# Optimization experiments

Hardware: AMD Instinct MI355X
Metric: run time of the kernel (lower is better)

Reference implementation:

```python
import jax, jax.numpy as jnp
import numpy as np

B, C, NNEG, D = 4096, 5, 20, 128
NUM_EMB = 400000  # vocab * num_poly


def setup_inputs() -> dict:
    key = jax.random.key(0)
    k1, k2, k3, k4, k5 = jax.random.split(key, 5)
    iword = jax.random.randint(k1, (B,), 0, NUM_EMB, dtype=jnp.int64)
    owords = jax.random.randint(k2, (B, C), 0, NUM_EMB, dtype=jnp.int64)
    nwords = jax.random.randint(k3, (B, C * NNEG), 0, NUM_EMB, dtype=jnp.int64)
    emb1 = jax.random.normal(k4, (NUM_EMB, D), dtype=jnp.float32) * 0.1
    emb2 = jax.random.normal(k5, (NUM_EMB, D), dtype=jnp.float32) * 0.1
    return {"iword": iword, "owords": owords, "nwords": nwords,
            "emb1": emb1, "emb2": emb2}


def reference(iword, owords, nwords, emb1, emb2):
    v1 = emb1[iword]          # [B, D] center vectors
    v2 = emb2[owords]         # [B, C, D] context vectors
    vn = emb2[nwords]         # [B, C*NNEG, D] negative vectors
    # positive: mean over context of log sigmoid(v2 . v1)
    o_scores = jnp.einsum('bcd,bd->bc', v2, v1)
    oloss = jax.nn.log_sigmoid(o_scores).mean(axis=1)              # [B]
    # negatives: vectors are negated -> log sigmoid(-score), sum over negs, mean over context
    n_scores = jnp.einsum('bkd,bd->bk', vn, v1)                    # [B, C*NNEG]
    nloss = jax.nn.log_sigmoid(-n_scores).reshape(-1, C, NNEG).sum(axis=2).mean(axis=1)  # [B]
    return -(oloss + nloss).mean()
```

## Files before the change

### kernel.cpp

```cpp
#include <hip/hip_runtime.h>
#include <math.h>

#define B 4096
#define C 5
#define NNEG 20
#define D 128
#define NROWS (C + C * NNEG)
#define NSLOT 14

__device__ __forceinline__ float log_sigmoid(float x) {
    return fminf(x, 0.0f) - log1pf(__expf(-fabsf(x)));
}

__global__ __launch_bounds__(256) void sgns_partial(
    const int* __restrict__ iword,
    const int* __restrict__ owords,
    const int* __restrict__ nwords,
    const float* __restrict__ emb1,
    const float* __restrict__ emb2,
    float* __restrict__ partial)
{
    const int b    = blockIdx.x;
    const int tid  = threadIdx.x;
    const int lane = tid & 63;
    const int wave = tid >> 6;
    const int hw   = tid >> 5;
    const int l32  = tid & 31;

    const float4* v1p = (const float4*)(emb1 + (long)iword[b] * D);
    const float4 v1f = v1p[l32];

    int   rIdx[NSLOT];
    float sgn[NSLOT];
    bool  valid[NSLOT];
    #pragma unroll
    for (int s = 0; s < NSLOT; ++s) {
        const int r = s * 8 + hw;
        valid[s] = (r < NROWS);
        const int rr = valid[s] ? r : 0;
        const bool pos = (rr < C);
        sgn[s] = pos ? 1.0f : -1.0f;
        rIdx[s] = pos ? owords[b * C + rr]
                      : nwords[b * (C * NNEG) + (rr - C)];
    }

    float4 rw[NSLOT];
    #pragma unroll
    for (int s = 0; s < NSLOT; ++s) {
        rw[s] = ((const float4*)(emb2 + (long)rIdx[s] * D))[l32];
    }

    float acc = 0.0f;
    #pragma unroll
    for (int s = 0; s < NSLOT; ++s) {
        float t = v1f.x * rw[s].x + v1f.y * rw[s].y
                + v1f.z * rw[s].z + v1f.w * rw[s].w;
        t += __shfl_xor(t, 1, 64);
        t += __shfl_xor(t, 2, 64);
        t += __shfl_xor(t, 4, 64);
        t += __shfl_xor(t, 8, 64);
        t += __shfl_xor(t, 16, 64);
        const float v = log_sigmoid(sgn[s] * t);
        acc += valid[s] ? v : 0.0f;
    }

    acc += __shfl_xor(acc, 32, 64);

    __shared__ float wsum[4];
    if (lane == 0) wsum[wave] = acc;
    __syncthreads();
    if (tid == 0)
        partial[b] = wsum[0] + wsum[1] + wsum[2] + wsum[3];
}

__global__ __launch_bounds__(256) void sgns_reduce(
    const float* __restrict__ partial,
    float* __restrict__ out)
{
    const int tid = threadIdx.x;
    float acc = 0.0f;
    for (int i = tid; i < B; i += 256) acc += partial[i];

    #pragma unroll
    for (int off = 32; off > 0; off >>= 1)
        acc += __shfl_xor(acc, off, 64);

    __shared__ float ws[4];
    if ((tid & 63) == 0) ws[tid >> 6] = acc;
    __syncthreads();
    if (tid == 0) out[0] = -(ws[0] + ws[1] + ws[2] + ws[3]) / (float)(B * C);
}

extern "C" void kernel_launch(void* const* d_in, const int* in_sizes, int n_in,
                              void* d_out, int out_size, void* d_ws, size_t ws_size,
                              hipStream_t stream) {
    const int*   iword  = (const int*)d_in[0];
    const int*   owords = (const int*)d_in[1];
    const int*   nwords = (const int*)d_in[2];
    const float* emb1   = (const float*)d_in[3];
    const float* emb2   = (const float*)d_in[4];
    float* out     = (float*)d_out;
    float* partial = (float*)d_ws;

    sgns_partial<<<B, 256, 0, stream>>>(iword, owords, nwords, emb1, emb2, partial);
    sgns_reduce<<<1, 256, 0, stream>>>(partial, out);
}
```

Measured before the change: 361.2 us.

## Invert embedding gather into bucketed sequential stream over emb2 rows

Replaces the per-sample random gather of emb2 rows with a multi-kernel pipeline. First the center vectors are copied into a compact buffer. Then every (sample, row) lookup is scattered by atomics into per-row buckets of capacity 8, with an overflow list for rows that exceed it. Finally the whole emb2 table is streamed sequentially with one-row-ahead prefetch, and each row is dotted against the center vectors that requested it, with log-sigmoid and reductions done in separate kernels. This trades scattered HBM reads for a coalesced full-table scan, at the cost of atomics, extra launches and a score buffer. It falls back to the old gather when the workspace is too small.

```diff
diff --git a/kernel.cpp b/kernel.cpp
--- a/kernel.cpp
+++ b/kernel.cpp
@@ -6,64 +6,147 @@
 #define NNEG 20
 #define D 128
 #define NROWS (C + C * NNEG)
-#define NSLOT 14
+#define NEMB 400000
+#define CAP 8
+#define OVF_MAX 8192
+#define RPB 200
+#define SBLK (NEMB / RPB)
+#define NIT (RPB / 8)
+
+typedef unsigned int uint32;
+
+#define OFF_V1     ((size_t)0)
+#define OFF_SCORE  (OFF_V1 + (size_t)B * D * 4)
+#define OFF_PART   (OFF_SCORE + (size_t)B * NROWS * 4)
+#define OFF_CNT    (OFF_PART + (size_t)B * 4)
+#define OFF_OVFC   (OFF_CNT + (size_t)NEMB * 4)
+#define OFF_OVF    (OFF_OVFC + 64)
+#define OFF_BUCKET (OFF_OVF + (size_t)OVF_MAX * 8)
+#define WS_NEED    (OFF_BUCKET + (size_t)NEMB * CAP * 4)
 
 __device__ __forceinline__ float log_sigmoid(float x) {
     return fminf(x, 0.0f) - log1pf(__expf(-fabsf(x)));
 }
 
-__global__ __launch_bounds__(256) void sgns_partial(
-    const int* __restrict__ iword,
-    const int* __restrict__ owords,
-    const int* __restrict__ nwords,
-    const float* __restrict__ emb1,
-    const float* __restrict__ emb2,
-    float* __restrict__ partial)
-{
-    const int b    = blockIdx.x;
-    const int tid  = threadIdx.x;
-    const int lane = tid & 63;
-    const int wave = tid >> 6;
-    const int hw   = tid >> 5;
-    const int l32  = tid & 31;
-
-    const float4* v1p = (const float4*)(emb1 + (long)iword[b] * D);
-    const float4 v1f = v1p[l32];
-
-    int   rIdx[NSLOT];
-    float sgn[NSLOT];
-    bool  valid[NSLOT];
-    #pragma unroll
-    for (int s = 0; s < NSLOT; ++s) {
-        const int r = s * 8 + hw;
-        valid[s] = (r < NROWS);
-        const int rr = valid[s] ? r : 0;
-        const bool pos = (rr < C);
-        sgn[s] = pos ? 1.0f : -1.0f;
-        rIdx[s] = pos ? owords[b * C + rr]
-                      : nwords[b * (C * NNEG) + (rr - C)];
-    }
-
-    float4 rw[NSLOT];
-    #pragma unroll
-    for (int s = 0; s < NSLOT; ++s) {
-        rw[s] = ((const float4*)(emb2 + (long)rIdx[s] * D))[l32];
-    }
+__device__ __forceinline__ float dot_butterfly(float4 vf, float4 rv) {
+    float t = vf.x * rv.x + vf.y * rv.y + vf.z * rv.z + vf.w * rv.w;
+    t += __shfl_xor(t, 1, 64);
+    t += __shfl_xor(t, 2, 64);
+    t += __shfl_xor(t, 4, 64);
+    t += __shfl_xor(t, 8, 64);
+    t += __shfl_xor(t, 16, 64);
+    return t;
+}
+
+__global__ __launch_bounds__(256) void kA_init(const int* __restrict__ iword,
+                                               const float* __restrict__ emb1,
+                                               float* __restrict__ v1s,
+                                               uint32* __restrict__ cnt,
+                                               uint32* __restrict__ ovfc) {
+    const int g = blockIdx.x * 256 + threadIdx.x;
+    for (int i = g; i < NEMB; i += 512 * 256) cnt[i] = 0;
+    if (g == 0) *ovfc = 0;
+
+    const int hw = threadIdx.x >> 5, l32 = threadIdx.x & 31;
+    const int b = blockIdx.x * 8 + hw;
+    int ci = iword[b];
+    if ((unsigned)ci >= NEMB) ci = 0;
+    const float4 v = ((const float4*)(emb1 + (long)ci * D))[l32];
+    ((float4*)(v1s + (long)b * D))[l32] = v;
+}
+
+__global__ __launch_bounds__(128) void k2_scatter(const int* __restrict__ ow,
+                                                  const int* __restrict__ nw,
+                                                  uint32* __restrict__ cnt,
+                                                  uint32* __restrict__ bucket,
+                                                  uint32* __restrict__ ovfc,
+                                                  uint32* __restrict__ ovf) {
+    const int b = blockIdx.x;
+    const int r = threadIdx.x;
+    if (r >= NROWS) return;
+    int row = (r < C) ? ow[b * C + r] : nw[b * (C * NNEG) + (r - C)];
+    if ((unsigned)row >= NEMB) row = 0;
+    const uint32 pair = ((uint32)b << 7) | (uint32)r;
+    const uint32 c = atomicAdd(&cnt[row], 1u);
+    if (c < CAP) {
+        bucket[(long)row * CAP + c] = pair;
+    } else {
+        const uint32 o = atomicAdd(ovfc, 1u);
+        if (o < OVF_MAX) { ovf[2 * o] = (uint32)row; ovf[2 * o + 1] = pair; }
+    }
+}
+
+__global__ __launch_bounds__(256) void k3_stream(const float* __restrict__ emb2,
+                                                 const float* __restrict__ v1s,
+                                                 const uint32* __restrict__ cnt,
+                                                 const uint32* __restrict__ bucket,
+                                                 const uint32* __restrict__ ovfc,
+                                                 const uint32* __restrict__ ovf,
+                                                 float* __restrict__ score) {
+    const int tid = threadIdx.x;
+    const int hw = tid >> 5, l32 = tid & 31;
+    const int rbase = blockIdx.x * RPB;
+
+    int    row_c = rbase + hw;
+    float4 rv_c  = ((const float4*)(emb2 + (long)row_c * D))[l32];
+    uint32 n_c   = cnt[row_c];
+    uint32 bw_c  = bucket[(long)row_c * CAP + (l32 & 7)];
+
+    #pragma unroll 1
+    for (int i = 0; i < NIT; ++i) {
+        const int row_n = (i + 1 < NIT) ? (row_c + 8) : row_c;
+        const float4 rv_n = ((const float4*)(emb2 + (long)row_n * D))[l32];
+        const uint32 n_n  = cnt[row_n];
+        const uint32 bw_n = bucket[(long)row_n * CAP + (l32 & 7)];
+
+        if (n_c) {
+            uint32 n = n_c > CAP ? CAP : n_c;
+            for (uint32 k = 0; k < n; ++k) {
+                const uint32 pair = __shfl(bw_c, (int)k, 32);
+                const int bb = (int)(pair >> 7);
+                const int rr = (int)(pair & 127);
+                const float4 vf = ((const float4*)(v1s + (long)bb * D))[l32];
+                const float t = dot_butterfly(vf, rv_c);
+                if (l32 == 0 && bb < B && rr < NROWS) score[bb * NROWS + rr] = t;
+            }
+        }
+        row_c = row_n; rv_c = rv_n; n_c = n_n; bw_c = bw_n;
+    }
+
+    if (blockIdx.x == 0) {
+        uint32 m = *ovfc;
+        if (m > OVF_MAX) m = OVF_MAX;
+        for (uint32 e = hw; e < m; e += 8) {
+            uint32 row = ovf[2 * e];
+            const uint32 pair = ovf[2 * e + 1];
+            if (row >= NEMB) continue;
+            const int bb = (int)(pair >> 7);
+            const int rr = (int)(pair & 127);
+            const float4 rv = ((const float4*)(emb2 + (long)row * D))[l32];
+            const float4 vf = ((const float4*)(v1s + (long)bb * D))[l32];
+            const float t = dot_butterfly(vf, rv);
+            if (l32 == 0 && bb < B && rr < NROWS) score[bb * NROWS + rr] = t;
+        }
+    }
+}
+
+__global__ __launch_bounds__(256) void k5_finish(const float* __restrict__ score,
+                                                 float* __restrict__ partial) {
+    const int b = blockIdx.x;
+    const int tid = threadIdx.x;
+    const int lane = tid & 63, wave = tid >> 6, hw = tid >> 5;
 
     float acc = 0.0f;
     #pragma unroll
-    for (int s = 0; s < NSLOT; ++s) {
-        float t = v1f.x * rw[s].x + v1f.y * rw[s].y
-                + v1f.z * rw[s].z + v1f.w * rw[s].w;
-        t += __shfl_xor(t, 1, 64);
-        t += __shfl_xor(t, 2, 64);
-        t += __shfl_xor(t, 4, 64);
-        t += __shfl_xor(t, 8, 64);
-        t += __shfl_xor(t, 16, 64);
-        const float v = log_sigmoid(sgn[s] * t);
-        acc += valid[s] ? v : 0.0f;
-    }
-
+    for (int s = 0; s < 14; ++s) {
+        const int r = s * 8 + hw;
+        const bool valid = (r < NROWS);
+        const int rr = valid ? r : 0;
+        const float sgn = (rr < C) ? 1.0f : -1.0f;
+        const float t = score[b * NROWS + rr];
+        const float v = log_sigmoid(sgn * t);
+        acc += valid ? v : 0.0f;
+    }
     acc += __shfl_xor(acc, 32, 64);
 
     __shared__ float wsum[4];
@@ -73,22 +156,46 @@
         partial[b] = wsum[0] + wsum[1] + wsum[2] + wsum[3];
 }
 
-__global__ __launch_bounds__(256) void sgns_reduce(
-    const float* __restrict__ partial,
-    float* __restrict__ out)
-{
+__global__ __launch_bounds__(256) void sgns_reduce(const float* __restrict__ partial,
+                                                   float* __restrict__ out) {
     const int tid = threadIdx.x;
     float acc = 0.0f;
     for (int i = tid; i < B; i += 256) acc += partial[i];
-
     #pragma unroll
     for (int off = 32; off > 0; off >>= 1)
         acc += __shfl_xor(acc, off, 64);
-
     __shared__ float ws[4];
     if ((tid & 63) == 0) ws[tid >> 6] = acc;
     __syncthreads();
     if (tid == 0) out[0] = -(ws[0] + ws[1] + ws[2] + ws[3]) / (float)(B * C);
+}
+
+__global__ __launch_bounds__(256) void sgns_partial_gather(
+    const int* __restrict__ iword, const int* __restrict__ owords,
+    const int* __restrict__ nwords, const float* __restrict__ emb1,
+    const float* __restrict__ emb2, float* __restrict__ partial)
+{
+    const int b = blockIdx.x, tid = threadIdx.x;
+    const int lane = tid & 63, wave = tid >> 6, hw = tid >> 5, l32 = tid & 31;
+    const float4 v1f = ((const float4*)(emb1 + (long)iword[b] * D))[l32];
+    float acc = 0.0f;
+    #pragma unroll
+    for (int s = 0; s < 14; ++s) {
+        const int r = s * 8 + hw;
+        const bool valid = (r < NROWS);
+        const int rr = valid ? r : 0;
+        const bool pos = (rr < C);
+        const int idx = pos ? owords[b * C + rr] : nwords[b * (C * NNEG) + (rr - C)];
+        const float4 rv = ((const float4*)(emb2 + (long)idx * D))[l32];
+        const float t = dot_butterfly(v1f, rv);
+        const float v = log_sigmoid((pos ? 1.0f : -1.0f) * t);
+        acc += valid ? v : 0.0f;
+    }
+    acc += __shfl_xor(acc, 32, 64);
+    __shared__ float wsum[4];
+    if (lane == 0) wsum[wave] = acc;
+    __syncthreads();
+    if (tid == 0) partial[b] = wsum[0] + wsum[1] + wsum[2] + wsum[3];
 }
 
 extern "C" void kernel_launch(void* const* d_in, const int* in_sizes, int n_in,
@@ -99,9 +206,26 @@
     const int*   nwords = (const int*)d_in[2];
     const float* emb1   = (const float*)d_in[3];
     const float* emb2   = (const float*)d_in[4];
-    float* out     = (float*)d_out;
-    float* partial = (float*)d_ws;
-
-    sgns_partial<<<B, 256, 0, stream>>>(iword, owords, nwords, emb1, emb2, partial);
-    sgns_reduce<<<1, 256, 0, stream>>>(partial, out);
-}
+    float* out = (float*)d_out;
+
+    char* ws = (char*)d_ws;
+    float*  v1s     = (float*)(ws + OFF_V1);
+    float*  score   = (float*)(ws + OFF_SCORE);
+    float*  partial = (float*)(ws + OFF_PART);
+    uint32* cnt     = (uint32*)(ws + OFF_CNT);
+    uint32* ovfc    = (uint32*)(ws + OFF_OVFC);
+    uint32* ovf     = (uint32*)(ws + OFF_OVF);
+    uint32* bucket  = (uint32*)(ws + OFF_BUCKET);
+
+    if (ws_size >= WS_NEED) {
+        kA_init   <<<512, 256, 0, stream>>>(iword, emb1, v1s, cnt, ovfc);
+        k2_scatter<<<B, 128, 0, stream>>>(owords, nwords, cnt, bucket, ovfc, ovf);
+        k3_stream <<<SBLK, 256, 0, stream>>>(emb2, v1s, cnt, bucket, ovfc, ovf, score);
+        k5_finish <<<B, 256, 0, stream>>>(score, partial);
+        sgns_reduce<<<1, 256, 0, stream>>>(partial, out);
+    } else {
+        float* part2 = (float*)d_ws;
+        sgns_partial_gather<<<B, 256, 0, stream>>>(iword, owords, nwords, emb1, emb2, part2);
+        sgns_reduce<<<1, 256, 0, stream>>>(part2, out);
+    }
+}
```

New measurement: 450.1 us. 24.6% more time.
